# Optimization experiments

Hardware: AMD Instinct MI355X
Metric: run time of the kernel (lower is better)

## Reference

```python
import jax, jax.numpy as jnp
import numpy as np

HEADS = 4

def _dwconv(x, w, pad):
    # depthwise conv, NCHW, kernel [C,1,k,k]
    return jax.lax.conv_general_dilated(
        x, w, window_strides=(1, 1), padding=((pad, pad), (pad, pad)),
        feature_group_count=x.shape[1],
        dimension_numbers=('NCHW', 'OIHW', 'NCHW'))

def _l2norm(t):
    # matches torch F.normalize(dim=-1, eps=1e-12)
    n = jnp.sqrt(jnp.sum(t * t, axis=-1, keepdims=True))
    return t / jnp.maximum(n, 1e-12)

def _reshape_attn(q, k, v, temp, if_box):
    b, c, hw0 = q.shape
    factor = HEADS
    ch = c // HEADS
    pad = (-hw0) % factor

    def prep(t):
        t = jnp.pad(t, ((0, 0), (0, 0), (0, pad)))
        hw = t.shape[-1] // factor
        if if_box:  # 'b (head c) (factor hw) -> b head (c factor) hw'
            t = t.reshape(b, HEADS, ch, factor, hw)
        else:       # 'b (head c) (hw factor) -> b head (c factor) hw'
            t = t.reshape(b, HEADS, ch, hw, factor).transpose(0, 1, 2, 4, 3)
        return t.reshape(b, HEADS, ch * factor, hw)

    qq, kk, vv = prep(q), prep(k), prep(v)
    qq, kk = _l2norm(qq), _l2norm(kk)
    attn = jnp.einsum('bhdn,bhen->bhde', qq, kk) * temp  # temp [heads,1,1]
    e = jnp.exp(attn)
    attn = e / (jnp.sum(e, axis=-1, keepdims=True) + 1.0)  # softmax_1
    o = jnp.einsum('bhde,bhen->bhdn', attn, vv)
    hw = o.shape[-1]
    if if_box:
        o = o.reshape(b, HEADS, ch, factor, hw).reshape(b, c, factor * hw)
    else:
        o = o.reshape(b, HEADS, ch, factor, hw).transpose(0, 1, 2, 4, 3).reshape(b, c, hw * factor)
    return o[:, :, :hw0]

def _conv1x1(x, w):
    return jnp.einsum('bchw,oc->bohw', x, w)

def _forward(x, temperature, w_qkv, w_dw3, w_dw5, w_dw7, w_fuse, b_fuse, w_proj):
    b, c, h, w = x.shape
    ch = c // 2
    # sort first half of channels along h then w
    xh = x[:, :ch]
    idx_h = jnp.argsort(xh, axis=-2)
    xs = jnp.take_along_axis(xh, idx_h, axis=-2)
    idx_w = jnp.argsort(xs, axis=-1)
    xs = jnp.take_along_axis(xs, idx_w, axis=-1)
    x = jnp.concatenate([xs, x[:, ch:]], axis=1)

    q = _conv1x1(x, w_qkv)  # [b,5c,h,w]
    cat = jnp.concatenate([_dwconv(q, w_dw3, 1), _dwconv(q, w_dw5, 2), _dwconv(q, w_dw7, 3)], axis=1)
    qkv = _conv1x1(cat, w_fuse) + b_fuse[None, :, None, None]
    q1, k1, q2, k2, v = jnp.split(qkv, 5, axis=1)

    hw = h * w
    vf = v.reshape(b, c, hw)
    idx = jnp.argsort(vf, axis=-1)
    vs = jnp.take_along_axis(vf, idx, axis=-1)
    gat = lambda t: jnp.take_along_axis(t.reshape(b, c, hw), idx, axis=-1)

    out1 = _reshape_attn(gat(q1), gat(k1), vs, temperature, True)
    out2 = _reshape_attn(gat(q2), gat(k2), vs, temperature, False)

    inv = jnp.argsort(idx, axis=-1)  # scatter(out, 2, idx, out) == unsort
    out1 = jnp.take_along_axis(out1, inv, axis=-1).reshape(b, c, h, w)
    out2 = jnp.take_along_axis(out2, inv, axis=-1).reshape(b, c, h, w)

    out = _conv1x1(out1 * out2, w_proj)
    r = out[:, :ch]
    r = jnp.take_along_axis(r, jnp.argsort(idx_w, axis=-1), axis=-1)
    r = jnp.take_along_axis(r, jnp.argsort(idx_h, axis=-2), axis=-2)
    return jnp.concatenate([r, out[:, ch:]], axis=1)

def setup_inputs() -> dict:
    key = jax.random.key(0)
    ks = jax.random.split(key, 8)
    b, c, h, w = 2, 64, 192, 192
    x = jax.random.normal(ks[0], (b, c, h, w), jnp.float32)
    temperature = jnp.ones((HEADS, 1, 1), jnp.float32)
    w_qkv = jax.random.normal(ks[1], (5 * c, c), jnp.float32) * 0.05
    w_dw3 = jax.random.normal(ks[2], (5 * c, 1, 3, 3), jnp.float32) * 0.1
    w_dw5 = jax.random.normal(ks[3], (5 * c, 1, 5, 5), jnp.float32) * 0.05
    w_dw7 = jax.random.normal(ks[4], (5 * c, 1, 7, 7), jnp.float32) * 0.03
    w_fuse = jax.random.normal(ks[5], (5 * c, 15 * c), jnp.float32) * 0.02
    b_fuse = jnp.zeros((5 * c,), jnp.float32)
    w_proj = jax.random.normal(ks[6], (c, c), jnp.float32) * 0.05
    return {'x': x, 'temperature': temperature, 'w_qkv': w_qkv, 'w_dw3': w_dw3,
            'w_dw5': w_dw5, 'w_dw7': w_dw7, 'w_fuse': w_fuse, 'b_fuse': b_fuse,
            'w_proj': w_proj}

def reference(x, temperature, w_qkv, w_dw3, w_dw5, w_dw7, w_fuse, b_fuse, w_proj):
    return _forward(x, temperature, w_qkv, w_dw3, w_dw5, w_dw7, w_fuse, b_fuse, w_proj)
```

## Files before the change

kernel.cpp:

```cpp
#include <hip/hip_runtime.h>
#include <stdint.h>
#include <stddef.h>

constexpr int IMH = 192;
constexpr int IMW = 192;
constexpr int HW  = 36864;
constexpr int BB  = 2;
constexpr int CC  = 64;
constexpr int CHF = 32;
constexpr int C5  = 320;
constexpr int NQ  = 9216;
constexpr int CROWS = 64;
constexpr int CHWN  = CROWS * IMW;
constexpr int NCHUNK = 32;
constexpr int CHN = HW / 4 / NCHUNK;
constexpr int NSEG = 12;
constexpr int SEGN = HW / NSEG;
constexpr int NBIN = 2048;

typedef float fx2 __attribute__((ext_vector_type(2)));
typedef float fx4 __attribute__((ext_vector_type(4)));
typedef _Float16 f16;
typedef _Float16 f16x8 __attribute__((ext_vector_type(8)));
typedef float f32x4 __attribute__((ext_vector_type(4)));

static __device__ __forceinline__ uint32_t f2s(float f) {
    uint32_t u = __float_as_uint(f);
    return (u & 0x80000000u) ? ~u : (u | 0x80000000u);
}
static __device__ __forceinline__ float s2f(uint32_t s) {
    uint32_t u = (s & 0x80000000u) ? (s & 0x7FFFFFFFu) : ~s;
    return __uint_as_float(u);
}

static __device__ void bitonic256(uint64_t* keys, int tid) {
    for (unsigned k = 2; k <= 256; k <<= 1) {
        for (unsigned j = k >> 1; j; j >>= 1) {
            __syncthreads();
            unsigned i = ((tid & ~(j - 1)) << 1) | (tid & (j - 1));
            unsigned p = i | j;
            bool up = ((i & k) == 0);
            uint64_t a = keys[i], b = keys[p];
            if ((a > b) == up) { keys[i] = b; keys[p] = a; }
        }
    }
    __syncthreads();
}

__global__ __launch_bounds__(128) void k_sort_h(const float* __restrict__ x, float* __restrict__ A,
                                                int* __restrict__ idx_h) {
    __shared__ uint64_t keys[256];
    int tid = threadIdx.x;
    int blk = blockIdx.x;
    int w = blk % IMW;
    int c = (blk / IMW) % CHF;
    int b = blk / (IMW * CHF);
    const float* col = x + ((size_t)(b * CC) + c) * HW + w;
    for (int i = tid; i < 256; i += 128)
        keys[i] = (i < IMH) ? ((((uint64_t)f2s(col[(size_t)i * IMW])) << 32) | (uint32_t)i) : ~0ull;
    bitonic256(keys, tid);
    float* ocol = A + ((size_t)(b * CC) + c) * HW + w;
    int* icol = idx_h + ((size_t)(b * CHF) + c) * HW + w;
    for (int i = tid; i < IMH; i += 128) {
        uint64_t k = keys[i];
        ocol[(size_t)i * IMW] = s2f((uint32_t)(k >> 32));
        icol[(size_t)i * IMW] = (int)(k & 0xFFFFFFFFull);
    }
}

__global__ __launch_bounds__(128) void k_sort_w(float* __restrict__ A, int* __restrict__ idx_w) {
    __shared__ uint64_t keys[256];
    int tid = threadIdx.x;
    int blk = blockIdx.x;
    int h = blk % IMH;
    int c = (blk / IMH) % CHF;
    int b = blk / (IMH * CHF);
    float* row = A + ((size_t)(b * CC) + c) * HW + (size_t)h * IMW;
    for (int i = tid; i < 256; i += 128)
        keys[i] = (i < IMW) ? ((((uint64_t)f2s(row[i])) << 32) | (uint32_t)i) : ~0ull;
    bitonic256(keys, tid);
    int* irow = idx_w + ((size_t)(b * CHF) + c) * HW + (size_t)h * IMW;
    for (int i = tid; i < IMW; i += 128) {
        uint64_t k = keys[i];
        row[i] = s2f((uint32_t)(k >> 32));
        irow[i] = (int)(k & 0xFFFFFFFFull);
    }
}

__global__ __launch_bounds__(256) void k_gemm_q(const float* __restrict__ wq, const float* __restrict__ A,
                                                const float* __restrict__ x, float* __restrict__ q) {
    __shared__ float Wt[64][68];
    __shared__ float Xt[64][68];
    int tid = threadIdx.x;
    int n0 = blockIdx.x * 64, m0 = blockIdx.y * 64, b = blockIdx.z;
    for (int l = 0; l < 16; ++l) {
        int idx = l * 256 + tid;
        int cc = idx & 63, m = idx >> 6;
        Wt[cc][m] = wq[(size_t)(m0 + m) * 64 + cc];
    }
    for (int l = 0; l < 16; ++l) {
        int idx = l * 256 + tid;
        int n = idx & 63, cc = idx >> 6;
        const float* sp = (cc < CHF) ? A : x;
        Xt[cc][n] = sp[((size_t)(b * CC) + cc) * HW + n0 + n];
    }
    __syncthreads();
    int ty = tid >> 4, tx = tid & 15;
    float acc[4][4] = {};
    for (int cc = 0; cc < 64; ++cc) {
        float4 av = *(const float4*)&Wt[cc][ty * 4];
        float4 bv = *(const float4*)&Xt[cc][tx * 4];
        float aa[4] = {av.x, av.y, av.z, av.w};
        float bb[4] = {bv.x, bv.y, bv.z, bv.w};
        #pragma unroll
        for (int i = 0; i < 4; ++i)
            #pragma unroll
            for (int j = 0; j < 4; ++j)
                acc[i][j] = fmaf(aa[i], bb[j], acc[i][j]);
    }
    for (int i = 0; i < 4; ++i) {
        float4 o;
        o.x = acc[i][0]; o.y = acc[i][1]; o.z = acc[i][2]; o.w = acc[i][3];
        *(float4*)&q[((size_t)(b * C5) + m0 + ty * 4 + i) * HW + n0 + tx * 4] = o;
    }
}

template <int KS>
__global__ __launch_bounds__(256) void k_dwconv(const float* __restrict__ q, const float* __restrict__ wd,
                                                float* __restrict__ slice, int r0) {
    constexpr int PAD = KS / 2;
    constexpr int EXT = 32 + 2 * PAD;
    __shared__ float tile[EXT][EXT];
    int tid = threadIdx.x;
    int b = blockIdx.z, c = blockIdx.y;
    int t = blockIdx.x;
    int ty0 = r0 + (t / 6) * 32, tx0 = (t % 6) * 32;
    const float* src = q + ((size_t)(b * C5) + c) * HW;
    for (int i = tid; i < EXT * EXT; i += 256) {
        int iy = i / EXT, ix = i % EXT;
        int gy = ty0 + iy - PAD, gx = tx0 + ix - PAD;
        float v = 0.f;
        if (gy >= 0 && gy < IMH && gx >= 0 && gx < IMW) v = src[gy * IMW + gx];
        tile[iy][ix] = v;
    }
    __syncthreads();
    float wreg[KS * KS];
    #pragma unroll
    for (int i = 0; i < KS * KS; ++i) wreg[i] = wd[(size_t)c * KS * KS + i];
    float* dst = slice + ((size_t)(b * C5) + c) * CHWN;
    #pragma unroll
    for (int k = 0; k < 4; ++k) {
        int pix = k * 256 + tid;
        int py = pix >> 5, px = pix & 31;
        float acc = 0.f;
        #pragma unroll
        for (int ky = 0; ky < KS; ++ky)
            #pragma unroll
            for (int kx = 0; kx < KS; ++kx)
                acc = fmaf(tile[py + ky][px + kx], wreg[ky * KS + kx], acc);
        dst[(ty0 - r0 + py) * IMW + tx0 + px] = acc;
    }
}

__global__ __launch_bounds__(256) void k_gemm_fuse(const float* __restrict__ wf,
                                                   const float* __restrict__ slice, const float* __restrict__ bias,
                                                   float* __restrict__ qkvI, float* __restrict__ qkvV,
                                                   int g, int r0) {
    __shared__ f16 Ah[64][40];
    __shared__ f16 Al[64][40];
    int tid = threadIdx.x;
    int n0 = blockIdx.x * 128, py = blockIdx.y, m0 = py * 64, b = blockIdx.z;
    int lane = tid & 63, wv = tid >> 6;
    int l15 = lane & 15, lg = lane >> 4;
    int nwave = n0 + wv * 32;
    int sm = tid >> 2, skr = (tid & 3) * 8;
    int gk = g * 320;
    f32x4 acc[4][2];
    #pragma unroll
    for (int i = 0; i < 4; ++i)
        #pragma unroll
        for (int j = 0; j < 2; ++j)
            acc[i][j] = (f32x4){0.f, 0.f, 0.f, 0.f};

    const float* xcol = slice + (size_t)(b * C5) * CHWN + nwave + l15;
    const float* wrow = wf + (size_t)(m0 + sm) * 960 + gk + skr;

    for (int k0 = 0; k0 < 320; k0 += 32) {
        if (k0) __syncthreads();
        {
            float4 w0 = *(const float4*)(wrow + k0);
            float4 w1 = *(const float4*)(wrow + k0 + 4);
            float wvv[8] = {w0.x, w0.y, w0.z, w0.w, w1.x, w1.y, w1.z, w1.w};
            f16x8 hv, lv;
            #pragma unroll
            for (int j = 0; j < 8; ++j) {
                f16 h = (f16)wvv[j];
                hv[j] = h;
                lv[j] = (f16)(wvv[j] - (float)h);
            }
            *(f16x8*)&Ah[sm][skr] = hv;
            *(f16x8*)&Al[sm][skr] = lv;
        }
        float xv[2][8];
        #pragma unroll
        for (int fn = 0; fn < 2; ++fn)
            #pragma unroll
            for (int j = 0; j < 8; ++j)
                xv[fn][j] = xcol[(size_t)(k0 + lg * 8 + j) * CHWN + fn * 16];
        __syncthreads();
        f16x8 bh[2], bl[2];
        #pragma unroll
        for (int fn = 0; fn < 2; ++fn)
            #pragma unroll
            for (int j = 0; j < 8; ++j) {
                float v = xv[fn][j];
                f16 h = (f16)v;
                bh[fn][j] = h;
                bl[fn][j] = (f16)(v - (float)h);
            }
        #pragma unroll
        for (int fm = 0; fm < 4; ++fm) {
            f16x8 ah = *(const f16x8*)&Ah[fm * 16 + l15][lg * 8];
            f16x8 al = *(const f16x8*)&Al[fm * 16 + l15][lg * 8];
            #pragma unroll
            for (int fn = 0; fn < 2; ++fn) {
                acc[fm][fn] = __builtin_amdgcn_mfma_f32_16x16x32_f16(ah, bh[fn], acc[fm][fn], 0, 0, 0);
                acc[fm][fn] = __builtin_amdgcn_mfma_f32_16x16x32_f16(ah, bl[fn], acc[fm][fn], 0, 0, 0);
                acc[fm][fn] = __builtin_amdgcn_mfma_f32_16x16x32_f16(al, bh[fn], acc[fm][fn], 0, 0, 0);
            }
        }
    }

    #pragma unroll
    for (int fm = 0; fm < 4; ++fm) {
        #pragma unroll
        for (int r = 0; r < 4; ++r) {
            int m = m0 + fm * 16 + lg * 4 + r;
            int cg = m & 63;
            size_t colb = (size_t)r0 * IMW + nwave + l15;
            if (py < 4) {
                float* bp = qkvI + ((size_t)(b * CC + cg) * HW) * 4 + py;
                if (g == 0) {
                    float bv = bias[m];
                    #pragma unroll
                    for (int fn = 0; fn < 2; ++fn)
                        bp[(colb + fn * 16) * 4] = acc[fm][fn][r] + bv;
                } else {
                    #pragma unroll
                    for (int fn = 0; fn < 2; ++fn)
                        bp[(colb + fn * 16) * 4] += acc[fm][fn][r];
                }
            } else {
                float* bp = qkvV + (size_t)(b * CC + cg) * HW;
                if (g == 0) {
                    float bv = bias[m];
                    #pragma unroll
                    for (int fn = 0; fn < 2; ++fn)
                        bp[colb + fn * 16] = acc[fm][fn][r] + bv;
                } else {
                    #pragma unroll
                    for (int fn = 0; fn < 2; ++fn)
                        bp[colb + fn * 16] += acc[fm][fn][r];
                }
            }
        }
    }
}

template <int FIRST>
__global__ __launch_bounds__(256) void k_rcount(const uint64_t* __restrict__ in, const float* __restrict__ qkvv,
                                                uint32_t* __restrict__ cntG, int shift) {
    __shared__ uint32_t hist[NBIN];
    int t = threadIdx.x;
    int seg = blockIdx.x, row = blockIdx.y;
    #pragma unroll
    for (int k = 0; k < NBIN / 256; ++k) hist[k * 256 + t] = 0;
    __syncthreads();
    if (FIRST) {
        const float* srcf = qkvv + (size_t)row * HW + (size_t)seg * SEGN;
        #pragma unroll
        for (int i = 0; i < SEGN / 256; ++i) {
            unsigned d = f2s(srcf[i * 256 + t]) & (NBIN - 1);
            atomicAdd(&hist[d], 1u);
        }
    } else {
        const uint64_t* src = in + (size_t)row * HW + (size_t)seg * SEGN;
        #pragma unroll
        for (int i = 0; i < SEGN / 256; ++i) {
            unsigned d = (unsigned)(src[i * 256 + t] >> shift) & (NBIN - 1);
            atomicAdd(&hist[d], 1u);
        }
    }
    __syncthreads();
    uint32_t* dstc = cntG + ((size_t)row * NSEG + seg) * NBIN;
    #pragma unroll
    for (int k = 0; k < NBIN / 256; ++k) dstc[k * 256 + t] = hist[k * 256 + t];
}

__global__ __launch_bounds__(256) void k_rscan(uint32_t* __restrict__ cntG) {
    __shared__ uint32_t tot[NBIN];
    __shared__ uint32_t gsum[256];
    __shared__ uint32_t gbase[256];
    int t = threadIdx.x;
    int row = blockIdx.x;
    uint32_t* base = cntG + (size_t)row * NSEG * NBIN;
    uint32_t loc = 0;
    #pragma unroll
    for (int k = 0; k < NBIN / 256; ++k) {
        int bn = t * (NBIN / 256) + k;
        uint32_t s = 0;
        for (int sg = 0; sg < NSEG; ++sg) s += base[sg * NBIN + bn];
        tot[bn] = s;
        loc += s;
    }
    gsum[t] = loc;
    __syncthreads();
    if (t == 0) {
        uint32_t acc = 0;
        for (int i = 0; i < 256; ++i) { uint32_t v = gsum[i]; gbase[i] = acc; acc += v; }
    }
    __syncthreads();
    uint32_t run = gbase[t];
    #pragma unroll
    for (int k = 0; k < NBIN / 256; ++k) {
        int bn = t * (NBIN / 256) + k;
        uint32_t tv = tot[bn];
        uint32_t r2 = run;
        for (int sg = 0; sg < NSEG; ++sg) {
            uint32_t cv = base[sg * NBIN + bn];
            base[sg * NBIN + bn] = r2;
            r2 += cv;
        }
        run += tv;
    }
}

template <int MODE>
__global__ __launch_bounds__(256) void k_rscatter(const uint64_t* __restrict__ in, const float* __restrict__ qkvv,
                                                  uint64_t* __restrict__ out, float* __restrict__ vso,
                                                  int* __restrict__ idxo, const uint32_t* __restrict__ cntG,
                                                  int shift) {
    __shared__ uint16_t wcnt[4][NBIN];
    __shared__ uint32_t runbase[NBIN];
    int t = threadIdx.x;
    int w = t >> 6, lane = t & 63;
    int seg = blockIdx.x, row = blockIdx.y;
    const uint32_t* cbase = cntG + ((size_t)row * NSEG + seg) * NBIN;
    #pragma unroll
    for (int k = 0; k < NBIN / 256; ++k) runbase[k * 256 + t] = cbase[k * 256 + t];
    for (int i = 0; i < SEGN / 256; ++i) {
        __syncthreads();
        #pragma unroll
        for (int k = 0; k < NBIN / 256; ++k)
            ((uint64_t*)wcnt)[k * 256 + t] = 0;
        __syncthreads();
        uint64_t kv;
        if (MODE == 1) {
            const float* srcf = qkvv + (size_t)row * HW + (size_t)seg * SEGN;
            kv = (((uint64_t)f2s(srcf[i * 256 + t])) << 32) | (uint32_t)(seg * SEGN + i * 256 + t);
        } else {
            const uint64_t* src = in + (size_t)row * HW + (size_t)seg * SEGN;
            kv = src[i * 256 + t];
        }
        unsigned d = (unsigned)(kv >> shift) & (NBIN - 1);
        uint64_t peers = ~0ull;
        #pragma unroll
        for (int bit = 0; bit < 11; ++bit) {
            uint64_t bm = __ballot((d >> bit) & 1u);
            peers &= ((d >> bit) & 1u) ? bm : ~bm;
        }
        unsigned lanerank = (unsigned)__popcll(peers & ((1ull << lane) - 1ull));
        unsigned wtotal = (unsigned)__popcll(peers);
        if (lanerank == 0) wcnt[w][d] = (uint16_t)wtotal;
        __syncthreads();
        unsigned wpre = 0;
        #pragma unroll
        for (int ww = 0; ww < 4; ++ww) {
            unsigned cv = wcnt[ww][d];
            if (ww < w) wpre += cv;
        }
        unsigned pos = runbase[d] + wpre + lanerank;
        if (MODE == 2) {
            vso[(size_t)row * HW + pos] = s2f((uint32_t)(kv >> 32));
            idxo[(size_t)row * HW + pos] = (int)(kv & 0xFFFFFFFFull);
        } else {
            out[(size_t)row * HW + pos] = kv;
        }
        __syncthreads();
        #pragma unroll
        for (int k = 0; k < NBIN / 256; ++k) {
            int bn = k * 256 + t;
            runbase[bn] += (uint32_t)wcnt[0][bn] + wcnt[1][bn] + wcnt[2][bn] + wcnt[3][bn];
        }
    }
}

__global__ __launch_bounds__(1024) void k_gather4(const int* __restrict__ idxv, const float* __restrict__ qkvI,
                                                  float* __restrict__ g4) {
    int i = blockIdx.x;
    int row = (i & 7) * 16 + ((i >> 3) & 15);
    int jh = i >> 7;
    const int* irow = idxv + (size_t)row * HW + jh * (HW / 2);
    size_t S4 = (size_t)BB * CC * HW;
    int tid = threadIdx.x;
    const fx4* src = (const fx4*)(qkvI + (size_t)row * HW * 4);
    size_t dbase = (size_t)row * HW + jh * (HW / 2);
    float* d0 = g4 + dbase;
    float* d1 = d0 + S4;
    float* d2 = d0 + 2 * S4;
    float* d3 = d0 + 3 * S4;
    #pragma unroll 3
    for (int s = 0; s < 9; ++s) {
        int j = s * 2048 + tid * 2;
        int2 p = *(const int2*)&irow[j];
        fx4 a = src[p.x];
        fx4 b4 = src[p.y];
        fx2 w0 = {a.x, b4.x};
        fx2 w1 = {a.y, b4.y};
        fx2 w2 = {a.z, b4.z};
        fx2 w3 = {a.w, b4.w};
        __builtin_nontemporal_store(w0, (fx2*)&d0[j]);
        __builtin_nontemporal_store(w1, (fx2*)&d1[j]);
        __builtin_nontemporal_store(w2, (fx2*)&d2[j]);
        __builtin_nontemporal_store(w3, (fx2*)&d3[j]);
    }
}

__global__ __launch_bounds__(256) void k_attn_qk(const float* __restrict__ g4,
                                                 float* __restrict__ partS, float* __restrict__ partN) {
    __shared__ float Qs[16][68];
    __shared__ float Ks[16][68];
    __shared__ float nqs[4][64];
    __shared__ float nks[4][64];
    int tid = threadIdx.x;
    int ychunk = blockIdx.x;
    int z = blockIdx.y;
    int vi = z & 1, hh = (z >> 1) & 3, b = z >> 3;
    size_t S4 = (size_t)BB * CC * HW;
    const float* Q = g4 + (vi ? 2 * S4 : (size_t)0);
    const float* Kp = g4 + (vi ? 3 * S4 : S4);
    int ty = tid >> 4, tx = tid & 15;
    float acc[4][4] = {};
    float nq = 0.f, nk = 0.f;
    int d0 = tid & 63, kset = tid >> 6;
    int nbase0 = ychunk * CHN;
    for (int it = 0; it < CHN / 16; ++it) {
        int nb0 = nbase0 + it * 16;
        __syncthreads();
        #pragma unroll
        for (int l = 0; l < 4; ++l) {
            int idx = l * 256 + tid;
            int d = idx >> 4, kk = idx & 15;
            int n = nb0 + kk;
            int cch = hh * 16 + (d >> 2), f = d & 3;
            size_t off = ((size_t)(b * CC) + cch) * HW + (vi ? (size_t)(n * 4 + f) : (size_t)(f * NQ + n));
            Qs[kk][d] = Q[off];
            Ks[kk][d] = Kp[off];
        }
        __syncthreads();
        #pragma unroll
        for (int kk = 0; kk < 16; ++kk) {
            float4 av = *(const float4*)&Qs[kk][ty * 4];
            float4 bv = *(const float4*)&Ks[kk][tx * 4];
            float aa[4] = {av.x, av.y, av.z, av.w};
            float bb[4] = {bv.x, bv.y, bv.z, bv.w};
            #pragma unroll
            for (int i = 0; i < 4; ++i)
                #pragma unroll
                for (int j = 0; j < 4; ++j)
                    acc[i][j] = fmaf(aa[i], bb[j], acc[i][j]);
        }
        #pragma unroll
        for (int kk2 = 0; kk2 < 4; ++kk2) {
            float qv = Qs[kset * 4 + kk2][d0];
            float kv = Ks[kset * 4 + kk2][d0];
            nq = fmaf(qv, qv, nq);
            nk = fmaf(kv, kv, nk);
        }
    }
    size_t sb = ((size_t)z * NCHUNK + ychunk) * 4096;
    #pragma unroll
    for (int i = 0; i < 4; ++i)
        #pragma unroll
        for (int j = 0; j < 4; ++j)
            partS[sb + (size_t)(ty * 4 + i) * 64 + tx * 4 + j] = acc[i][j];
    nqs[kset][d0] = nq;
    nks[kset][d0] = nk;
    __syncthreads();
    if (tid < 64) {
        float sq = nqs[0][tid] + nqs[1][tid] + nqs[2][tid] + nqs[3][tid];
        float sk = nks[0][tid] + nks[1][tid] + nks[2][tid] + nks[3][tid];
        size_t nb2 = ((size_t)z * NCHUNK + ychunk) * 128;
        partN[nb2 + tid] = sq;
        partN[nb2 + 64 + tid] = sk;
    }
}

__global__ __launch_bounds__(256) void k_attn_softmax(const float* __restrict__ partS,
                                                      const float* __restrict__ partN,
                                                      const float* __restrict__ temp, float* __restrict__ attnT) {
    __shared__ float nqv[64], nkv[64];
    __shared__ float pbuf[64][65];
    __shared__ float rred[64][4];
    __shared__ float rsum[64];
    int tid = threadIdx.x;
    int z = blockIdx.x;
    int hh = (z >> 1) & 3;
    if (tid < 128) {
        float s = 0.f;
        for (int ch = 0; ch < NCHUNK; ++ch) s += partN[((size_t)z * NCHUNK + ch) * 128 + tid];
        float nv = fmaxf(sqrtf(s), 1e-12f);
        if (tid < 64) nqv[tid] = nv; else nkv[tid - 64] = nv;
    }
    __syncthreads();
    float tf = temp[hh];
    int d = tid >> 2, qq = tid & 3;
    float psum = 0.f;
    for (int e = qq * 16; e < qq * 16 + 16; ++e) {
        float s = 0.f;
        for (int ch = 0; ch < NCHUNK; ++ch) s += partS[((size_t)z * NCHUNK + ch) * 4096 + (size_t)d * 64 + e];
        float p = expf(tf * s / (nqv[d] * nkv[e]));
        pbuf[d][e] = p;
        psum += p;
    }
    rred[d][qq] = psum;
    __syncthreads();
    if (tid < 64) rsum[tid] = rred[tid][0] + rred[tid][1] + rred[tid][2] + rred[tid][3] + 1.0f;
    __syncthreads();
    for (int e = qq * 16; e < qq * 16 + 16; ++e)
        attnT[(size_t)z * 4096 + (size_t)e * 64 + d] = pbuf[d][e] / rsum[d];
}

__global__ __launch_bounds__(256) void k_attn_av(const float* __restrict__ attnT, const float* __restrict__ vs,
                                                 float* __restrict__ O1, float* __restrict__ O2) {
    __shared__ float at_s[4096];
    int tid = threadIdx.x;
    int z = blockIdx.y;
    int vi = z & 1, hh = (z >> 1) & 3, b = z >> 3;
    for (int l = 0; l < 16; ++l) at_s[l * 256 + tid] = attnT[(size_t)z * 4096 + l * 256 + tid];
    __syncthreads();
    int n = blockIdx.x * 256 + tid;
    float acc[64];
    #pragma unroll
    for (int d = 0; d < 64; ++d) acc[d] = 0.f;
    for (int e = 0; e < 64; ++e) {
        int cch = hh * 16 + (e >> 2), f = e & 3;
        size_t p = vi ? (size_t)(n * 4 + f) : (size_t)(f * NQ + n);
        float vv = vs[((size_t)(b * CC) + cch) * HW + p];
        const float* ar = &at_s[e * 64];
        #pragma unroll
        for (int d4 = 0; d4 < 16; ++d4) {
            float4 a4 = *(const float4*)&ar[d4 * 4];
            acc[d4 * 4 + 0] = fmaf(a4.x, vv, acc[d4 * 4 + 0]);
            acc[d4 * 4 + 1] = fmaf(a4.y, vv, acc[d4 * 4 + 1]);
            acc[d4 * 4 + 2] = fmaf(a4.z, vv, acc[d4 * 4 + 2]);
            acc[d4 * 4 + 3] = fmaf(a4.w, vv, acc[d4 * 4 + 3]);
        }
    }
    float* Ob = vi ? O2 : O1;
    #pragma unroll
    for (int d = 0; d < 64; ++d) {
        int cch = hh * 16 + (d >> 2), f = d & 3;
        size_t p = vi ? (size_t)(n * 4 + f) : (size_t)(f * NQ + n);
        Ob[((size_t)(b * CC) + cch) * HW + p] = acc[d];
    }
}

__global__ void k_prod_scatter(const float* __restrict__ O1, const float* __restrict__ O2,
                               const int* __restrict__ idxv, float* __restrict__ pu) {
    int j = blockIdx.x * 256 + threadIdx.x;
    int row = blockIdx.y;
    size_t o = (size_t)row * HW + j;
    int p = idxv[o];
    pu[(size_t)row * HW + p] = O1[o] * O2[o];
}

__global__ __launch_bounds__(256) void k_gemm_proj(const float* __restrict__ wp, const float* __restrict__ pu,
                                                   float* __restrict__ op) {
    __shared__ float wt[2048];
    int tid = threadIdx.x;
    int mh = blockIdx.y, b = blockIdx.z;
    for (int l = 0; l < 8; ++l) {
        int i = l * 256 + tid;
        int mm = i >> 6, c = i & 63;
        wt[c * 32 + mm] = wp[(size_t)(mh * 32 + mm) * 64 + c];
    }
    __syncthreads();
    int n = blockIdx.x * 256 + tid;
    float acc[32];
    #pragma unroll
    for (int m = 0; m < 32; ++m) acc[m] = 0.f;
    const float* src = pu + (size_t)(b * CC) * HW + n;
    for (int c = 0; c < 64; ++c) {
        float xv = src[(size_t)c * HW];
        const float* wr = &wt[c * 32];
        #pragma unroll
        for (int m4 = 0; m4 < 8; ++m4) {
            float4 w4 = *(const float4*)&wr[m4 * 4];
            acc[m4 * 4 + 0] = fmaf(w4.x, xv, acc[m4 * 4 + 0]);
            acc[m4 * 4 + 1] = fmaf(w4.y, xv, acc[m4 * 4 + 1]);
            acc[m4 * 4 + 2] = fmaf(w4.z, xv, acc[m4 * 4 + 2]);
            acc[m4 * 4 + 3] = fmaf(w4.w, xv, acc[m4 * 4 + 3]);
        }
    }
    float* dst = op + ((size_t)(b * CC) + mh * 32) * HW + n;
    for (int m = 0; m < 32; ++m) dst[(size_t)m * HW] = acc[m];
}

__global__ void k_final(const float* __restrict__ op, const int* __restrict__ idx_h,
                        const int* __restrict__ idx_w, float* __restrict__ out) {
    int i = blockIdx.x * 256 + threadIdx.x;
    int p = i % HW;
    int c = (i / HW) % CC;
    int b = i / (HW * CC);
    float v = op[i];
    if (c < CHF) {
        int h = p / IMW, w = p % IMW;
        size_t ib = ((size_t)(b * CHF) + c) * HW;
        int W0 = idx_w[ib + h * IMW + w];
        int H0 = idx_h[ib + h * IMW + W0];
        out[((size_t)(b * CC) + c) * HW + H0 * IMW + W0] = v;
    } else {
        out[i] = v;
    }
}

extern "C" void kernel_launch(void* const* d_in, const int* in_sizes, int n_in,
                              void* d_out, int out_size, void* d_ws, size_t ws_size,
                              hipStream_t stream) {
    (void)in_sizes; (void)n_in; (void)out_size; (void)ws_size;
    const float* x    = (const float*)d_in[0];
    const float* temp = (const float*)d_in[1];
    const float* wq   = (const float*)d_in[2];
    const float* wd3  = (const float*)d_in[3];
    const float* wd5  = (const float*)d_in[4];
    const float* wd7  = (const float*)d_in[5];
    const float* wf   = (const float*)d_in[6];
    const float* bf   = (const float*)d_in[7];
    const float* wp   = (const float*)d_in[8];
    float* out = (float*)d_out;
    float* ws = (float*)d_ws;

    int*      idx_h = (int*)(ws + 0);
    int*      idx_w = (int*)(ws + 2359296);
    float*    A     = ws + 4718592;
    float*    slice = ws + 4718592;
    float*    q     = ws + 12582912;
    float*    qkvI  = ws + 36175872;
    float*    qkvV  = ws + 55050240;
    int*      idxv  = (int*)(ws + 4718592);
    uint32_t* cntG  = (uint32_t*)(ws + 9437184);
    uint64_t* keyA  = (uint64_t*)(ws + 12582912);
    uint64_t* keyB  = (uint64_t*)(ws + 22020096);
    float*    vs    = ws + 31457280;
    float*    g4    = ws + 12582912;
    float*    O1    = ws + 36175872;
    float*    O2    = ws + 40894464;
    float*    pu    = ws + 45613056;
    float*    op    = ws + 50331648;
    float*    partS = ws + 55050240;
    float*    partN = ws + 57147392;
    float*    attnT = ws + 57212928;

    k_sort_h<<<12288, 128, 0, stream>>>(x, A, idx_h);
    k_sort_w<<<12288, 128, 0, stream>>>(A, idx_w);
    k_gemm_q<<<dim3(576, 5, 2), 256, 0, stream>>>(wq, A, x, q);

    for (int g = 0; g < 3; ++g) {
        for (int chunk = 0; chunk < 3; ++chunk) {
            int r0 = chunk * CROWS;
            if (g == 0)      k_dwconv<3><<<dim3(12, 320, 2), 256, 0, stream>>>(q, wd3, slice, r0);
            else if (g == 1) k_dwconv<5><<<dim3(12, 320, 2), 256, 0, stream>>>(q, wd5, slice, r0);
            else             k_dwconv<7><<<dim3(12, 320, 2), 256, 0, stream>>>(q, wd7, slice, r0);
            k_gemm_fuse<<<dim3(96, 5, 2), 256, 0, stream>>>(wf, slice, bf, qkvI, qkvV, g, r0);
        }
    }

    k_rcount<1><<<dim3(NSEG, 128), 256, 0, stream>>>(nullptr, qkvV, cntG, 32);
    k_rscan<<<128, 256, 0, stream>>>(cntG);
    k_rscatter<1><<<dim3(NSEG, 128), 256, 0, stream>>>(nullptr, qkvV, keyB, nullptr, nullptr, cntG, 32);
    k_rcount<0><<<dim3(NSEG, 128), 256, 0, stream>>>(keyB, nullptr, cntG, 43);
    k_rscan<<<128, 256, 0, stream>>>(cntG);
    k_rscatter<0><<<dim3(NSEG, 128), 256, 0, stream>>>(keyB, nullptr, keyA, nullptr, nullptr, cntG, 43);
    k_rcount<0><<<dim3(NSEG, 128), 256, 0, stream>>>(keyA, nullptr, cntG, 54);
    k_rscan<<<128, 256, 0, stream>>>(cntG);
    k_rscatter<2><<<dim3(NSEG, 128), 256, 0, stream>>>(keyA, nullptr, nullptr, vs, idxv, cntG, 54);

    k_gather4<<<256, 1024, 0, stream>>>(idxv, qkvI, g4);

    k_attn_qk<<<dim3(NCHUNK, 16), 256, 0, stream>>>(g4, partS, partN);
    k_attn_softmax<<<16, 256, 0, stream>>>(partS, partN, temp, attnT);
    k_attn_av<<<dim3(36, 16), 256, 0, stream>>>(attnT, vs, O1, O2);

    k_prod_scatter<<<dim3(144, 128), 256, 0, stream>>>(O1, O2, idxv, pu);
    k_gemm_proj<<<dim3(144, 2, 2), 256, 0, stream>>>(wp, pu, op);
    k_final<<<18432, 256, 0, stream>>>(op, idx_h, idx_w, out);
}
```

Measured before the change: 1.207 ms.

## Batch 16 columns/rows per block in bitonic sort kernels with coalesced tile loads

Each sort block now handles 16 columns (or rows) at once in a padded shared-memory tile, with 256 threads each running 8 compare-exchanges per bitonic step. Previously each block sorted a single column with strided global loads. The new layout coalesces global reads and writes across 16 adjacent columns and cuts the block count 16-fold. The cost is higher shared-memory use (34 KB per block), which may reduce occupancy, and possible bank conflicts from 64-bit accesses.

New measurement: 1.198 ms. Within noise of the previous version (-0.7%).

```diff
diff --git a/kernel.cpp b/kernel.cpp
--- a/kernel.cpp
+++ b/kernel.cpp
@@ -33,57 +33,89 @@
     return __uint_as_float(u);
 }
 
-static __device__ void bitonic256(uint64_t* keys, int tid) {
+static __device__ __forceinline__ void bitonic256x16(uint64_t (*keys)[17], int tid) {
+    int wl = tid & 15;
+    int p0 = tid >> 4;
     for (unsigned k = 2; k <= 256; k <<= 1) {
         for (unsigned j = k >> 1; j; j >>= 1) {
             __syncthreads();
-            unsigned i = ((tid & ~(j - 1)) << 1) | (tid & (j - 1));
-            unsigned p = i | j;
-            bool up = ((i & k) == 0);
-            uint64_t a = keys[i], b = keys[p];
-            if ((a > b) == up) { keys[i] = b; keys[p] = a; }
-        }
-    }
-    __syncthreads();
-}
-
-__global__ __launch_bounds__(128) void k_sort_h(const float* __restrict__ x, float* __restrict__ A,
+            #pragma unroll
+            for (int it = 0; it < 8; ++it) {
+                unsigned pp = (unsigned)(p0 + it * 16);
+                unsigned i = ((pp & ~(j - 1)) << 1) | (pp & (j - 1));
+                unsigned q = i | j;
+                bool up = ((i & k) == 0);
+                uint64_t a = keys[i][wl], b = keys[q][wl];
+                if ((a > b) == up) { keys[i][wl] = b; keys[q][wl] = a; }
+            }
+        }
+    }
+    __syncthreads();
+}
+
+__global__ __launch_bounds__(256) void k_sort_h(const float* __restrict__ x, float* __restrict__ A,
                                                 int* __restrict__ idx_h) {
-    __shared__ uint64_t keys[256];
+    __shared__ uint64_t keys[256][17];
     int tid = threadIdx.x;
     int blk = blockIdx.x;
-    int w = blk % IMW;
-    int c = (blk / IMW) % CHF;
-    int b = blk / (IMW * CHF);
-    const float* col = x + ((size_t)(b * CC) + c) * HW + w;
-    for (int i = tid; i < 256; i += 128)
-        keys[i] = (i < IMH) ? ((((uint64_t)f2s(col[(size_t)i * IMW])) << 32) | (uint32_t)i) : ~0ull;
-    bitonic256(keys, tid);
-    float* ocol = A + ((size_t)(b * CC) + c) * HW + w;
-    int* icol = idx_h + ((size_t)(b * CHF) + c) * HW + w;
-    for (int i = tid; i < IMH; i += 128) {
-        uint64_t k = keys[i];
-        ocol[(size_t)i * IMW] = s2f((uint32_t)(k >> 32));
-        icol[(size_t)i * IMW] = (int)(k & 0xFFFFFFFFull);
-    }
-}
-
-__global__ __launch_bounds__(128) void k_sort_w(float* __restrict__ A, int* __restrict__ idx_w) {
-    __shared__ uint64_t keys[256];
+    int wt = blk % 12;
+    int c  = (blk / 12) % CHF;
+    int b  = blk / (12 * CHF);
+    int w0 = wt * 16;
+    const float* base = x + ((size_t)(b * CC) + c) * HW + w0;
+    #pragma unroll
+    for (int l = 0; l < 12; ++l) {
+        int idx = l * 256 + tid;
+        int h = idx >> 4, wl = idx & 15;
+        keys[h][wl] = (((uint64_t)f2s(base[(size_t)h * IMW + wl])) << 32) | (uint32_t)h;
+    }
+    #pragma unroll
+    for (int l = 0; l < 4; ++l) {
+        int idx = l * 256 + tid;
+        keys[192 + (idx >> 4)][idx & 15] = ~0ull;
+    }
+    bitonic256x16(keys, tid);
+    float* ocol = A + ((size_t)(b * CC) + c) * HW + w0;
+    int* icol = idx_h + ((size_t)(b * CHF) + c) * HW + w0;
+    #pragma unroll
+    for (int l = 0; l < 12; ++l) {
+        int idx = l * 256 + tid;
+        int h = idx >> 4, wl = idx & 15;
+        uint64_t kk = keys[h][wl];
+        ocol[(size_t)h * IMW + wl] = s2f((uint32_t)(kk >> 32));
+        icol[(size_t)h * IMW + wl] = (int)(kk & 0xFFFFFFFFull);
+    }
+}
+
+__global__ __launch_bounds__(256) void k_sort_w(float* __restrict__ A, int* __restrict__ idx_w) {
+    __shared__ uint64_t keys[256][17];
     int tid = threadIdx.x;
     int blk = blockIdx.x;
-    int h = blk % IMH;
-    int c = (blk / IMH) % CHF;
-    int b = blk / (IMH * CHF);
-    float* row = A + ((size_t)(b * CC) + c) * HW + (size_t)h * IMW;
-    for (int i = tid; i < 256; i += 128)
-        keys[i] = (i < IMW) ? ((((uint64_t)f2s(row[i])) << 32) | (uint32_t)i) : ~0ull;
-    bitonic256(keys, tid);
-    int* irow = idx_w + ((size_t)(b * CHF) + c) * HW + (size_t)h * IMW;
-    for (int i = tid; i < IMW; i += 128) {
-        uint64_t k = keys[i];
-        row[i] = s2f((uint32_t)(k >> 32));
-        irow[i] = (int)(k & 0xFFFFFFFFull);
+    int ht = blk % 12;
+    int c  = (blk / 12) % CHF;
+    int b  = blk / (12 * CHF);
+    int h0 = ht * 16;
+    float* base = A + ((size_t)(b * CC) + c) * HW + (size_t)h0 * IMW;
+    #pragma unroll
+    for (int l = 0; l < 12; ++l) {
+        int idx = l * 256 + tid;
+        int hl = idx / 192, w = idx % 192;
+        keys[w][hl] = (((uint64_t)f2s(base[(size_t)hl * IMW + w])) << 32) | (uint32_t)w;
+    }
+    #pragma unroll
+    for (int l = 0; l < 4; ++l) {
+        int idx = l * 256 + tid;
+        keys[192 + (idx >> 4)][idx & 15] = ~0ull;
+    }
+    bitonic256x16(keys, tid);
+    int* irow = idx_w + ((size_t)(b * CHF) + c) * HW + (size_t)h0 * IMW;
+    #pragma unroll
+    for (int l = 0; l < 12; ++l) {
+        int idx = l * 256 + tid;
+        int hl = idx / 192, w = idx % 192;
+        uint64_t kk = keys[w][hl];
+        base[(size_t)hl * IMW + w] = s2f((uint32_t)(kk >> 32));
+        irow[(size_t)hl * IMW + w] = (int)(kk & 0xFFFFFFFFull);
     }
 }
 
@@ -662,8 +694,8 @@
     float*    partN = ws + 57147392;
     float*    attnT = ws + 57212928;
 
-    k_sort_h<<<12288, 128, 0, stream>>>(x, A, idx_h);
-    k_sort_w<<<12288, 128, 0, stream>>>(A, idx_w);
+    k_sort_h<<<768, 256, 0, stream>>>(x, A, idx_h);
+    k_sort_w<<<768, 256, 0, stream>>>(A, idx_w);
     k_gemm_q<<<dim3(576, 5, 2), 256, 0, stream>>>(wq, A, x, q);
 
     for (int g = 0; g < 3; ++g) {
```
